# Kernel optimization log

Measured on AMD Instinct MI355X. Metric: run time of the kernel, lower is better.

Reference implementation:

```python
import jax, jax.numpy as jnp
import numpy as np

R = 1          # box filter radius -> 3x3 kernel
EPS = 0.01     # regularization


def _box_kernel(r, ch):
    k = 2 * r + 1
    return jnp.full((ch, 1, k, k), 1.0 / (k * k), dtype=jnp.float32)


def _box(x, kernel, groups):
    # depthwise box filter, stride 1, 'same' padding (NCHW)
    return jax.lax.conv_general_dilated(
        x, kernel, window_strides=(1, 1), padding='SAME',
        dimension_numbers=('NCHW', 'OIHW', 'NCHW'),
        feature_group_count=groups)


def setup_inputs() -> dict:
    key = jax.random.key(0)
    k1, k2 = jax.random.split(key)
    shape = (8, 3, 1024, 1024)
    return {
        'x': jax.random.normal(k1, shape, dtype=jnp.float32),
        'y': jax.random.normal(k2, shape, dtype=jnp.float32),
    }


def reference(x, y):
    _, C, H, W = x.shape
    kC = _box_kernel(R, C)   # per-channel depthwise kernel
    k1 = _box_kernel(R, 1)   # normalization kernel
    # N counts valid pixels under 'same' (zero) padding -> edge correction
    Nrm = _box(jnp.ones((1, 1, H, W), x.dtype), k1, 1)
    mean_x = _box(x, kC, C) / Nrm
    mean_y = _box(y, kC, C) / Nrm
    cov_xy = _box(x * y, kC, C) / Nrm - mean_x * mean_y
    var_x = _box(x * x, kC, C) / Nrm - mean_x * mean_x
    A = cov_xy / (var_x + EPS)
    b = mean_y - A * mean_x
    mean_A = _box(A, kC, C) / Nrm
    mean_b = _box(b, kC, C) / Nrm
    return mean_A * x + mean_b
```

## Files before the change

kernel.cpp:

```cpp
#include <hip/hip_runtime.h>


#define H 1024
#define W 1024
#define STRIP 32
#define WAVES 4
#define WVC 128

__global__ __launch_bounds__(256, 4) void gf_kernel(const float* __restrict__ xg,
                                                    const float* __restrict__ yg,
                                                    float* __restrict__ og)
{
    const int lane = threadIdx.x & 63;
    const int wv = threadIdx.x >> 6;
    const int c0 = blockIdx.x * WVC;
    const int R0 = (blockIdx.y * WAVES + wv) * STRIP;
    const size_t base = (size_t)blockIdx.z * (size_t)(H * W);
    const float* __restrict__ xp = xg + base;
    const float* __restrict__ yp = yg + base;
    float* __restrict__ op = og + base;

    const int colA = c0 + 2 * lane;
    const bool isL = (lane == 0);
    const bool isR = (lane == 63);
    const bool haloIn = isL ? (c0 > 0) : (isR ? (c0 + WVC < W) : false);
    const int hdelta = (isL ? (c0 - 2) : (c0 + WVC)) - colA;

    const float third = 1.0f / 3.0f;
    const float invcA = (colA == 0) ? 0.5f : third;
    const float invcB = (colA + 1 == W - 1) ? 0.5f : third;
    const float invcH = haloIn ? third : 0.0f;

    float hxA[3]={0,0,0}, hxB[3]={0,0,0}, hyA[3]={0,0,0}, hyB[3]={0,0,0};
    float hxxA[3]={0,0,0}, hxxB[3]={0,0,0}, hxyA[3]={0,0,0}, hxyB[3]={0,0,0};
    float hxH[3]={0,0,0}, hyH[3]={0,0,0}, hxxH[3]={0,0,0}, hxyH[3]={0,0,0};
    float hAA[3]={0,0,0}, hAB[3]={0,0,0}, hbA[3]={0,0,0}, hbB[3]={0,0,0};
    float xwA[3]={0,0,0}, xwB[3]={0,0,0};

    int off = (R0 - 2) * W + colA;

    float2 xv = {0,0}, yv = {0,0}, xh = {0,0}, yh = {0,0};
    if (R0 - 2 >= 0) {
        xv = *(const float2*)(xp + off);
        yv = *(const float2*)(yp + off);
        if (haloIn) {
            xh = *(const float2*)(xp + off + hdelta);
            yh = *(const float2*)(yp + off + hdelta);
        }
    }

#pragma unroll 3
    for (int s = 0; s < STRIP + 4; ++s) {
        const int lr = R0 - 2 + s;
        const int t = lr - 1;
        const int r = lr - 2;

        const int lrn = lr + 1;
        float2 xvN = {0,0}, yvN = {0,0}, xhN = {0,0}, yhN = {0,0};
        if (lrn >= 0 && lrn < H && s < STRIP + 3) {
            const int offn = off + W;
            xvN = *(const float2*)(xp + offn);
            yvN = *(const float2*)(yp + offn);
            if (haloIn) {
                xhN = *(const float2*)(xp + offn + hdelta);
                yhN = *(const float2*)(yp + offn + hdelta);
            }
        }

        const float xxA = xv.x * xv.x, xxB = xv.y * xv.y;
        const float xyA = xv.x * yv.x, xyB = xv.y * yv.y;
        float xl = __shfl_up(xv.y, 1, 64);
        float xr = __shfl_down(xv.x, 1, 64);
        float yl = __shfl_up(yv.y, 1, 64);
        float yr = __shfl_down(yv.x, 1, 64);
        xl = isL ? xh.y : xl;
        xr = isR ? xh.x : xr;
        yl = isL ? yh.y : yl;
        yr = isR ? yh.x : yr;

        hxA[0]=hxA[1]; hxA[1]=hxA[2];   hxB[0]=hxB[1]; hxB[1]=hxB[2];
        hyA[0]=hyA[1]; hyA[1]=hyA[2];   hyB[0]=hyB[1]; hyB[1]=hyB[2];
        hxxA[0]=hxxA[1]; hxxA[1]=hxxA[2]; hxxB[0]=hxxB[1]; hxxB[1]=hxxB[2];
        hxyA[0]=hxyA[1]; hxyA[1]=hxyA[2]; hxyB[0]=hxyB[1]; hxyB[1]=hxyB[2];
        hxH[0]=hxH[1]; hxH[1]=hxH[2];   hyH[0]=hyH[1]; hyH[1]=hyH[2];
        hxxH[0]=hxxH[1]; hxxH[1]=hxxH[2]; hxyH[0]=hxyH[1]; hxyH[1]=hxyH[2];

        const float sx = xv.x + xv.y;
        hxA[2] = xl + sx;   hxB[2] = sx + xr;
        const float sy = yv.x + yv.y;
        hyA[2] = yl + sy;   hyB[2] = sy + yr;
        const float sxx = xxA + xxB;
        hxxA[2] = fmaf(xl, xl, sxx);  hxxB[2] = fmaf(xr, xr, sxx);
        const float sxy = xyA + xyB;
        hxyA[2] = fmaf(xl, yl, sxy);  hxyB[2] = fmaf(xr, yr, sxy);

        const float selx  = isL ? xv.x : xv.y;
        const float sely  = isL ? yv.x : yv.y;
        const float selxx = isL ? xxA : xxB;
        const float selxy = isL ? xyA : xyB;
        hxH[2]  = xh.x + xh.y + selx;
        hyH[2]  = yh.x + yh.y + sely;
        hxxH[2] = fmaf(xh.x, xh.x, fmaf(xh.y, xh.y, selxx));
        hxyH[2] = fmaf(xh.x, yh.x, fmaf(xh.y, yh.y, selxy));

        const float rowfA = (t < 0 || t >= H) ? 0.0f
                          : ((t == 0 || t == H - 1) ? 0.5f : third);
        const float iA = rowfA * invcA;
        const float iB = rowfA * invcB;
        const float iH = rowfA * invcH;

        float AcA, bcA, AcB, bcB, Ah, bh;
        {
            const float mx  = (hxA[0] + hxA[1] + hxA[2]) * iA;
            const float my  = (hyA[0] + hyA[1] + hyA[2]) * iA;
            const float mxx = (hxxA[0] + hxxA[1] + hxxA[2]) * iA;
            const float mxy = (hxyA[0] + hxyA[1] + hxyA[2]) * iA;
            const float var = fmaf(-mx, mx, mxx);
            const float cov = fmaf(-mx, my, mxy);
            AcA = cov * __builtin_amdgcn_rcpf(var + 0.01f);
            bcA = fmaf(-AcA, mx, my);
        }
        {
            const float mx  = (hxB[0] + hxB[1] + hxB[2]) * iB;
            const float my  = (hyB[0] + hyB[1] + hyB[2]) * iB;
            const float mxx = (hxxB[0] + hxxB[1] + hxxB[2]) * iB;
            const float mxy = (hxyB[0] + hxyB[1] + hxyB[2]) * iB;
            const float var = fmaf(-mx, mx, mxx);
            const float cov = fmaf(-mx, my, mxy);
            AcB = cov * __builtin_amdgcn_rcpf(var + 0.01f);
            bcB = fmaf(-AcB, mx, my);
        }
        {
            const float mx  = (hxH[0] + hxH[1] + hxH[2]) * iH;
            const float my  = (hyH[0] + hyH[1] + hyH[2]) * iH;
            const float mxx = (hxxH[0] + hxxH[1] + hxxH[2]) * iH;
            const float mxy = (hxyH[0] + hxyH[1] + hxyH[2]) * iH;
            const float var = fmaf(-mx, mx, mxx);
            const float cov = fmaf(-mx, my, mxy);
            Ah = cov * __builtin_amdgcn_rcpf(var + 0.01f);
            bh = fmaf(-Ah, mx, my);
        }

        float Al = __shfl_up(AcB, 1, 64);
        float Ar = __shfl_down(AcA, 1, 64);
        float bl = __shfl_up(bcB, 1, 64);
        float br = __shfl_down(bcA, 1, 64);
        Al = isL ? Ah : Al;   Ar = isR ? Ah : Ar;
        bl = isL ? bh : bl;   br = isR ? bh : br;

        hAA[0]=hAA[1]; hAA[1]=hAA[2];  hAB[0]=hAB[1]; hAB[1]=hAB[2];
        hbA[0]=hbA[1]; hbA[1]=hbA[2];  hbB[0]=hbB[1]; hbB[1]=hbB[2];
        const float sA = AcA + AcB;
        hAA[2] = Al + sA;  hAB[2] = sA + Ar;
        const float sb = bcA + bcB;
        hbA[2] = bl + sb;  hbB[2] = sb + br;

        xwA[0]=xwA[1]; xwA[1]=xwA[2]; xwA[2]=xv.x;
        xwB[0]=xwB[1]; xwB[1]=xwB[2]; xwB[2]=xv.y;

        if (s >= 4) {
            const float rowfO = (r == 0 || r == H - 1) ? 0.5f : third;
            const float oA = rowfO * invcA;
            const float oB = rowfO * invcB;
            float2 o;
            o.x = fmaf((hAA[0] + hAA[1] + hAA[2]) * oA, xwA[0],
                       (hbA[0] + hbA[1] + hbA[2]) * oA);
            o.y = fmaf((hAB[0] + hAB[1] + hAB[2]) * oB, xwB[0],
                       (hbB[0] + hbB[1] + hbB[2]) * oB);
            *(float2*)(op + (off - 2 * W)) = o;
        }

        xv = xvN; yv = yvN; xh = xhN; yh = yhN;
        off += W;
    }
}

extern "C" void kernel_launch(void* const* d_in, const int* in_sizes, int n_in,
                              void* d_out, int out_size, void* d_ws, size_t ws_size,
                              hipStream_t stream) {
    const float* x = (const float*)d_in[0];
    const float* y = (const float*)d_in[1];
    float* out = (float*)d_out;
    const int planes = in_sizes[0] / (H * W);
    dim3 grid(W / WVC, H / (STRIP * WAVES), planes);
    gf_kernel<<<grid, dim3(256), 0, stream>>>(x, y, out);
}
```

Before: 263.2 us.

## Process four columns per lane with vertical-first running box sums

Each lane now handles four adjacent columns loaded as float4 instead of two as float2. The box filter becomes separable in the opposite order: vertical 3-row sums are kept as running partial sums, and only the vertical sums are exchanged across lanes for the horizontal pass. This removes the per-row sliding-window shifts and cuts shuffle and add work per pixel. The centre pixel is recovered from the running sums rather than kept in a window. STRIP drops to 16, WVC rises to 256 and the occupancy hint changes from 4 to 3, which increases the fraction of halo rows reloaded and adds register pressure; recovering x by subtraction can also introduce small rounding differences.

```diff
diff --git a/kernel.cpp b/kernel.cpp
--- a/kernel.cpp
+++ b/kernel.cpp
@@ -3,11 +3,11 @@
 
 #define H 1024
 #define W 1024
-#define STRIP 32
+#define STRIP 16
 #define WAVES 4
-#define WVC 128
-
-__global__ __launch_bounds__(256, 4) void gf_kernel(const float* __restrict__ xg,
+#define WVC 256
+
+__global__ __launch_bounds__(256, 3) void gf_kernel(const float* __restrict__ xg,
                                                     const float* __restrict__ yg,
                                                     float* __restrict__ og)
 {
@@ -20,154 +20,180 @@
     const float* __restrict__ yp = yg + base;
     float* __restrict__ op = og + base;
 
-    const int colA = c0 + 2 * lane;
+    const int colA = c0 + 4 * lane;
     const bool isL = (lane == 0);
     const bool isR = (lane == 63);
     const bool haloIn = isL ? (c0 > 0) : (isR ? (c0 + WVC < W) : false);
-    const int hdelta = (isL ? (c0 - 2) : (c0 + WVC)) - colA;
+    const int hoff = (isL ? (c0 - 2) : (c0 + WVC)) - colA;
 
     const float third = 1.0f / 3.0f;
-    const float invcA = (colA == 0) ? 0.5f : third;
-    const float invcB = (colA + 1 == W - 1) ? 0.5f : third;
+    float invc[4];
+    invc[0] = (colA == 0) ? 0.5f : third;
+    invc[1] = third;
+    invc[2] = third;
+    invc[3] = (colA + 3 == W - 1) ? 0.5f : third;
     const float invcH = haloIn ? third : 0.0f;
 
-    float hxA[3]={0,0,0}, hxB[3]={0,0,0}, hyA[3]={0,0,0}, hyB[3]={0,0,0};
-    float hxxA[3]={0,0,0}, hxxB[3]={0,0,0}, hxyA[3]={0,0,0}, hxyB[3]={0,0,0};
-    float hxH[3]={0,0,0}, hyH[3]={0,0,0}, hxxH[3]={0,0,0}, hxyH[3]={0,0,0};
-    float hAA[3]={0,0,0}, hAB[3]={0,0,0}, hbA[3]={0,0,0}, hbB[3]={0,0,0};
-    float xwA[3]={0,0,0}, xwB[3]={0,0,0};
+    float pX[4] = {0,0,0,0}, rX[4] = {0,0,0,0};
+    float pY[4] = {0,0,0,0}, rY[4] = {0,0,0,0};
+    float pXX[4] = {0,0,0,0}, rXX[4] = {0,0,0,0};
+    float pXY[4] = {0,0,0,0}, rXY[4] = {0,0,0,0};
+    float pHX[2] = {0,0}, rHX[2] = {0,0};
+    float pHY[2] = {0,0}, rHY[2] = {0,0};
+    float pHXX[2] = {0,0}, rHXX[2] = {0,0};
+    float pHXY[2] = {0,0}, rHXY[2] = {0,0};
+    float pA[4] = {0,0,0,0}, rA[4] = {0,0,0,0};
+    float pB[4] = {0,0,0,0}, rB[4] = {0,0,0,0};
+    float pAH = 0, rAH = 0, pBH = 0, rBH = 0;
 
     int off = (R0 - 2) * W + colA;
 
-    float2 xv = {0,0}, yv = {0,0}, xh = {0,0}, yh = {0,0};
+    float4 xv = {0,0,0,0}, yv = {0,0,0,0};
+    float2 xh = {0,0}, yh = {0,0};
     if (R0 - 2 >= 0) {
-        xv = *(const float2*)(xp + off);
-        yv = *(const float2*)(yp + off);
+        xv = *(const float4*)(xp + off);
+        yv = *(const float4*)(yp + off);
         if (haloIn) {
-            xh = *(const float2*)(xp + off + hdelta);
-            yh = *(const float2*)(yp + off + hdelta);
+            xh = *(const float2*)(xp + off + hoff);
+            yh = *(const float2*)(yp + off + hoff);
         }
     }
 
-#pragma unroll 3
+#pragma unroll 2
     for (int s = 0; s < STRIP + 4; ++s) {
         const int lr = R0 - 2 + s;
         const int t = lr - 1;
         const int r = lr - 2;
 
         const int lrn = lr + 1;
-        float2 xvN = {0,0}, yvN = {0,0}, xhN = {0,0}, yhN = {0,0};
-        if (lrn >= 0 && lrn < H && s < STRIP + 3) {
+        float4 xvN = {0,0,0,0}, yvN = {0,0,0,0};
+        float2 xhN = {0,0}, yhN = {0,0};
+        if ((unsigned)lrn < (unsigned)H && s < STRIP + 3) {
             const int offn = off + W;
-            xvN = *(const float2*)(xp + offn);
-            yvN = *(const float2*)(yp + offn);
+            xvN = *(const float4*)(xp + offn);
+            yvN = *(const float4*)(yp + offn);
             if (haloIn) {
-                xhN = *(const float2*)(xp + offn + hdelta);
-                yhN = *(const float2*)(yp + offn + hdelta);
-            }
-        }
-
-        const float xxA = xv.x * xv.x, xxB = xv.y * xv.y;
-        const float xyA = xv.x * yv.x, xyB = xv.y * yv.y;
-        float xl = __shfl_up(xv.y, 1, 64);
-        float xr = __shfl_down(xv.x, 1, 64);
-        float yl = __shfl_up(yv.y, 1, 64);
-        float yr = __shfl_down(yv.x, 1, 64);
-        xl = isL ? xh.y : xl;
-        xr = isR ? xh.x : xr;
-        yl = isL ? yh.y : yl;
-        yr = isR ? yh.x : yr;
-
-        hxA[0]=hxA[1]; hxA[1]=hxA[2];   hxB[0]=hxB[1]; hxB[1]=hxB[2];
-        hyA[0]=hyA[1]; hyA[1]=hyA[2];   hyB[0]=hyB[1]; hyB[1]=hyB[2];
-        hxxA[0]=hxxA[1]; hxxA[1]=hxxA[2]; hxxB[0]=hxxB[1]; hxxB[1]=hxxB[2];
-        hxyA[0]=hxyA[1]; hxyA[1]=hxyA[2]; hxyB[0]=hxyB[1]; hxyB[1]=hxyB[2];
-        hxH[0]=hxH[1]; hxH[1]=hxH[2];   hyH[0]=hyH[1]; hyH[1]=hyH[2];
-        hxxH[0]=hxxH[1]; hxxH[1]=hxxH[2]; hxyH[0]=hxyH[1]; hxyH[1]=hxyH[2];
-
-        const float sx = xv.x + xv.y;
-        hxA[2] = xl + sx;   hxB[2] = sx + xr;
-        const float sy = yv.x + yv.y;
-        hyA[2] = yl + sy;   hyB[2] = sy + yr;
-        const float sxx = xxA + xxB;
-        hxxA[2] = fmaf(xl, xl, sxx);  hxxB[2] = fmaf(xr, xr, sxx);
-        const float sxy = xyA + xyB;
-        hxyA[2] = fmaf(xl, yl, sxy);  hxyB[2] = fmaf(xr, yr, sxy);
-
-        const float selx  = isL ? xv.x : xv.y;
-        const float sely  = isL ? yv.x : yv.y;
-        const float selxx = isL ? xxA : xxB;
-        const float selxy = isL ? xyA : xyB;
-        hxH[2]  = xh.x + xh.y + selx;
-        hyH[2]  = yh.x + yh.y + sely;
-        hxxH[2] = fmaf(xh.x, xh.x, fmaf(xh.y, xh.y, selxx));
-        hxyH[2] = fmaf(xh.x, yh.x, fmaf(xh.y, yh.y, selxy));
-
-        const float rowfA = (t < 0 || t >= H) ? 0.0f
+                xhN = *(const float2*)(xp + offn + hoff);
+                yhN = *(const float2*)(yp + offn + hoff);
+            }
+        }
+
+        const float x_[4] = {xv.x, xv.y, xv.z, xv.w};
+        const float y_[4] = {yv.x, yv.y, yv.z, yv.w};
+        float vX[4], vY[4], vXX[4], vXY[4];
+#pragma unroll
+        for (int c = 0; c < 4; ++c) {
+            const float xx = x_[c] * x_[c];
+            const float xy = x_[c] * y_[c];
+            vX[c]  = pX[c]  + x_[c]; pX[c]  = rX[c]  + x_[c]; rX[c]  = x_[c];
+            vY[c]  = pY[c]  + y_[c]; pY[c]  = rY[c]  + y_[c]; rY[c]  = y_[c];
+            vXX[c] = pXX[c] + xx;    pXX[c] = rXX[c] + xx;    rXX[c] = xx;
+            vXY[c] = pXY[c] + xy;    pXY[c] = rXY[c] + xy;    rXY[c] = xy;
+        }
+        const float xh_[2] = {xh.x, xh.y};
+        const float yh_[2] = {yh.x, yh.y};
+        float vHX[2], vHY[2], vHXX[2], vHXY[2];
+#pragma unroll
+        for (int c = 0; c < 2; ++c) {
+            const float xx = xh_[c] * xh_[c];
+            const float xy = xh_[c] * yh_[c];
+            vHX[c]  = pHX[c]  + xh_[c]; pHX[c]  = rHX[c]  + xh_[c]; rHX[c]  = xh_[c];
+            vHY[c]  = pHY[c]  + yh_[c]; pHY[c]  = rHY[c]  + yh_[c]; rHY[c]  = yh_[c];
+            vHXX[c] = pHXX[c] + xx;     pHXX[c] = rHXX[c] + xx;     rHXX[c] = xx;
+            vHXY[c] = pHXY[c] + xy;     pHXY[c] = rHXY[c] + xy;     rHXY[c] = xy;
+        }
+
+        float lX  = __shfl_up(vX[3], 1, 64),  rXs  = __shfl_down(vX[0], 1, 64);
+        float lY  = __shfl_up(vY[3], 1, 64),  rYs  = __shfl_down(vY[0], 1, 64);
+        float lXX = __shfl_up(vXX[3], 1, 64), rXXs = __shfl_down(vXX[0], 1, 64);
+        float lXY = __shfl_up(vXY[3], 1, 64), rXYs = __shfl_down(vXY[0], 1, 64);
+        lX  = isL ? vHX[1]  : lX;   rXs  = isR ? vHX[0]  : rXs;
+        lY  = isL ? vHY[1]  : lY;   rYs  = isR ? vHY[0]  : rYs;
+        lXX = isL ? vHXX[1] : lXX;  rXXs = isR ? vHXX[0] : rXXs;
+        lXY = isL ? vHXY[1] : lXY;  rXYs = isR ? vHXY[0] : rXYs;
+
+        float hX[4], hY[4], hXX[4], hXY[4];
+        {
+            const float s01 = vX[0] + vX[1], s12 = vX[1] + vX[2], s23 = vX[2] + vX[3];
+            hX[0] = lX + s01; hX[1] = s01 + vX[2]; hX[2] = s12 + vX[3]; hX[3] = s23 + rXs;
+        }
+        {
+            const float s01 = vY[0] + vY[1], s12 = vY[1] + vY[2], s23 = vY[2] + vY[3];
+            hY[0] = lY + s01; hY[1] = s01 + vY[2]; hY[2] = s12 + vY[3]; hY[3] = s23 + rYs;
+        }
+        {
+            const float s01 = vXX[0] + vXX[1], s12 = vXX[1] + vXX[2], s23 = vXX[2] + vXX[3];
+            hXX[0] = lXX + s01; hXX[1] = s01 + vXX[2]; hXX[2] = s12 + vXX[3]; hXX[3] = s23 + rXXs;
+        }
+        {
+            const float s01 = vXY[0] + vXY[1], s12 = vXY[1] + vXY[2], s23 = vXY[2] + vXY[3];
+            hXY[0] = lXY + s01; hXY[1] = s01 + vXY[2]; hXY[2] = s12 + vXY[3]; hXY[3] = s23 + rXYs;
+        }
+
+        const float rowfA = ((unsigned)t >= (unsigned)H) ? 0.0f
                           : ((t == 0 || t == H - 1) ? 0.5f : third);
-        const float iA = rowfA * invcA;
-        const float iB = rowfA * invcB;
-        const float iH = rowfA * invcH;
-
-        float AcA, bcA, AcB, bcB, Ah, bh;
-        {
-            const float mx  = (hxA[0] + hxA[1] + hxA[2]) * iA;
-            const float my  = (hyA[0] + hyA[1] + hyA[2]) * iA;
-            const float mxx = (hxxA[0] + hxxA[1] + hxxA[2]) * iA;
-            const float mxy = (hxyA[0] + hxyA[1] + hxyA[2]) * iA;
+        float A_[4], B_[4];
+#pragma unroll
+        for (int c = 0; c < 4; ++c) {
+            const float ic  = rowfA * invc[c];
+            const float mx  = hX[c]  * ic;
+            const float my  = hY[c]  * ic;
+            const float mxx = hXX[c] * ic;
+            const float mxy = hXY[c] * ic;
             const float var = fmaf(-mx, mx, mxx);
             const float cov = fmaf(-mx, my, mxy);
-            AcA = cov * __builtin_amdgcn_rcpf(var + 0.01f);
-            bcA = fmaf(-AcA, mx, my);
-        }
-        {
-            const float mx  = (hxB[0] + hxB[1] + hxB[2]) * iB;
-            const float my  = (hyB[0] + hyB[1] + hyB[2]) * iB;
-            const float mxx = (hxxB[0] + hxxB[1] + hxxB[2]) * iB;
-            const float mxy = (hxyB[0] + hxyB[1] + hxyB[2]) * iB;
+            A_[c] = cov * __builtin_amdgcn_rcpf(var + 0.01f);
+            B_[c] = fmaf(-A_[c], mx, my);
+        }
+        float AH, BH;
+        {
+            const float iH  = rowfA * invcH;
+            const float hx  = vHX[0]  + vHX[1]  + (isL ? vX[0]  : vX[3]);
+            const float hy  = vHY[0]  + vHY[1]  + (isL ? vY[0]  : vY[3]);
+            const float hxx = vHXX[0] + vHXX[1] + (isL ? vXX[0] : vXX[3]);
+            const float hxy = vHXY[0] + vHXY[1] + (isL ? vXY[0] : vXY[3]);
+            const float mx  = hx * iH, my = hy * iH, mxx = hxx * iH, mxy = hxy * iH;
             const float var = fmaf(-mx, mx, mxx);
             const float cov = fmaf(-mx, my, mxy);
-            AcB = cov * __builtin_amdgcn_rcpf(var + 0.01f);
-            bcB = fmaf(-AcB, mx, my);
-        }
-        {
-            const float mx  = (hxH[0] + hxH[1] + hxH[2]) * iH;
-            const float my  = (hyH[0] + hyH[1] + hyH[2]) * iH;
-            const float mxx = (hxxH[0] + hxxH[1] + hxxH[2]) * iH;
-            const float mxy = (hxyH[0] + hxyH[1] + hxyH[2]) * iH;
-            const float var = fmaf(-mx, mx, mxx);
-            const float cov = fmaf(-mx, my, mxy);
-            Ah = cov * __builtin_amdgcn_rcpf(var + 0.01f);
-            bh = fmaf(-Ah, mx, my);
-        }
-
-        float Al = __shfl_up(AcB, 1, 64);
-        float Ar = __shfl_down(AcA, 1, 64);
-        float bl = __shfl_up(bcB, 1, 64);
-        float br = __shfl_down(bcA, 1, 64);
-        Al = isL ? Ah : Al;   Ar = isR ? Ah : Ar;
-        bl = isL ? bh : bl;   br = isR ? bh : br;
-
-        hAA[0]=hAA[1]; hAA[1]=hAA[2];  hAB[0]=hAB[1]; hAB[1]=hAB[2];
-        hbA[0]=hbA[1]; hbA[1]=hbA[2];  hbB[0]=hbB[1]; hbB[1]=hbB[2];
-        const float sA = AcA + AcB;
-        hAA[2] = Al + sA;  hAB[2] = sA + Ar;
-        const float sb = bcA + bcB;
-        hbA[2] = bl + sb;  hbB[2] = sb + br;
-
-        xwA[0]=xwA[1]; xwA[1]=xwA[2]; xwA[2]=xv.x;
-        xwB[0]=xwB[1]; xwB[1]=xwB[2]; xwB[2]=xv.y;
+            AH = cov * __builtin_amdgcn_rcpf(var + 0.01f);
+            BH = fmaf(-AH, mx, my);
+        }
+
+        float vA[4], vB[4];
+#pragma unroll
+        for (int c = 0; c < 4; ++c) {
+            vA[c] = pA[c] + A_[c]; pA[c] = rA[c] + A_[c]; rA[c] = A_[c];
+            vB[c] = pB[c] + B_[c]; pB[c] = rB[c] + B_[c]; rB[c] = B_[c];
+        }
+        const float vAH = pAH + AH;  pAH = rAH + AH;  rAH = AH;
+        const float vBH = pBH + BH;  pBH = rBH + BH;  rBH = BH;
+
+        float lA = __shfl_up(vA[3], 1, 64), rAs = __shfl_down(vA[0], 1, 64);
+        float lB = __shfl_up(vB[3], 1, 64), rBs = __shfl_down(vB[0], 1, 64);
+        lA = isL ? vAH : lA;  rAs = isR ? vAH : rAs;
+        lB = isL ? vBH : lB;  rBs = isR ? vBH : rBs;
 
         if (s >= 4) {
+            float hA[4], hB[4];
+            {
+                const float s01 = vA[0] + vA[1], s12 = vA[1] + vA[2], s23 = vA[2] + vA[3];
+                hA[0] = lA + s01; hA[1] = s01 + vA[2]; hA[2] = s12 + vA[3]; hA[3] = s23 + rAs;
+            }
+            {
+                const float s01 = vB[0] + vB[1], s12 = vB[1] + vB[2], s23 = vB[2] + vB[3];
+                hB[0] = lB + s01; hB[1] = s01 + vB[2]; hB[2] = s12 + vB[3]; hB[3] = s23 + rBs;
+            }
             const float rowfO = (r == 0 || r == H - 1) ? 0.5f : third;
-            const float oA = rowfO * invcA;
-            const float oB = rowfO * invcB;
-            float2 o;
-            o.x = fmaf((hAA[0] + hAA[1] + hAA[2]) * oA, xwA[0],
-                       (hbA[0] + hbA[1] + hbA[2]) * oA);
-            o.y = fmaf((hAB[0] + hAB[1] + hAB[2]) * oB, xwB[0],
-                       (hbB[0] + hbB[1] + hbB[2]) * oB);
-            *(float2*)(op + (off - 2 * W)) = o;
+            float4 o;
+            float o_[4];
+#pragma unroll
+            for (int c = 0; c < 4; ++c) {
+                const float oc = rowfO * invc[c];
+                const float xc = vX[c] - pX[c];
+                o_[c] = fmaf(hA[c] * oc, xc, hB[c] * oc);
+            }
+            o.x = o_[0]; o.y = o_[1]; o.z = o_[2]; o.w = o_[3];
+            *(float4*)(op + (off - 2 * W)) = o;
         }
 
         xv = xvN; yv = yvN; xh = xhN; yh = yhN;
```

New measurement: 253.8 us. 3.6% less time.
